# Kernel tuning notes

Measured on AMD Instinct MI355X. Metric: run time of the kernel, lower is better.

## Reference

```python
import jax, jax.numpy as jnp
import numpy as np

N, E, G, DIM = 100000, 1600000, 64, 128
BN_EPS = 1e-5


def setup_inputs() -> dict:
    key = jax.random.key(0)
    ks = jax.random.split(key, 20)
    inp = {
        "x": jax.random.normal(ks[0], (N, DIM), jnp.float32),
        "edge_attr": jax.random.normal(ks[1], (E, DIM), jnp.float32),
        "u": jax.random.normal(ks[2], (G, DIM), jnp.float32),
        "edge_index": jax.random.randint(ks[3], (2, E), 0, N, jnp.int32),
        "batch": jnp.sort(jax.random.randint(ks[4], (N,), 0, G, jnp.int32)),
    }
    # MLP params: layer 0 is Linear(3*DIM, DIM), layers 1,2 are Linear(DIM, DIM)
    def xavier(k, shape):
        fan_in, fan_out = shape[1], shape[0]
        lim = jnp.sqrt(6.0 / (fan_in + fan_out))
        return jax.random.uniform(k, shape, jnp.float32, -lim, lim)
    inp["W0"] = xavier(ks[5], (DIM, 3 * DIM)); inp["b0"] = jnp.zeros((DIM,), jnp.float32)
    inp["W1"] = xavier(ks[6], (DIM, DIM));     inp["b1"] = jnp.zeros((DIM,), jnp.float32)
    inp["W2"] = xavier(ks[7], (DIM, DIM));     inp["b2"] = jnp.zeros((DIM,), jnp.float32)
    for i in range(3):
        inp[f"g{i}"] = jnp.ones((DIM,), jnp.float32)   # BN gamma
        inp[f"bt{i}"] = jnp.zeros((DIM,), jnp.float32)  # BN beta
    return inp


def _bn(h, gamma, beta):
    # training-mode BatchNorm1d: batch mean, biased variance
    mu = jnp.mean(h, axis=0)
    var = jnp.var(h, axis=0)
    return (h - mu) * jax.lax.rsqrt(var + BN_EPS) * gamma + beta


def reference(x, edge_attr, u, W0, b0, W1, b1, W2, b2,
              g0, bt0, g1, bt1, g2, bt2, edge_index, batch):
    n = x.shape[0]
    src = edge_index[0]
    # scatter_mean(edge_attr, src) -> [N, DIM]
    sums = jax.ops.segment_sum(edge_attr, src, num_segments=n)
    cnt = jax.ops.segment_sum(jnp.ones((edge_attr.shape[0],), edge_attr.dtype),
                              src, num_segments=n)
    v_e = sums / jnp.maximum(cnt, 1.0)[:, None]
    out = jnp.concatenate([x, v_e, u[batch]], axis=1)  # [N, 3*DIM]
    for W, b, g, bt in ((W0, b0, g0, bt0), (W1, b1, g1, bt1), (W2, b2, g2, bt2)):
        out = jax.nn.relu(out @ W.T + b)
        out = _bn(out, g, bt)
        # dropout_rate = 0.0 -> identity
    return out
```

## Files before the change

### kernel.cpp

```cpp
#include <hip/hip_runtime.h>

#define DIMF 128
#define CAP 128

typedef __bf16 bf16x8 __attribute__((ext_vector_type(8)));
typedef float f32x4 __attribute__((ext_vector_type(4)));
typedef float f32x2 __attribute__((ext_vector_type(2)));

__device__ __forceinline__ unsigned short f2bf(float f) {
    union { float f; unsigned u; } v; v.f = f;
    unsigned r = v.u + 0x7FFFu + ((v.u >> 16) & 1u);
    return (unsigned short)(r >> 16);
}
__device__ __forceinline__ float bf2f(unsigned short h) {
    union { unsigned u; float f; } v; v.u = ((unsigned)h) << 16; return v.f;
}

__global__ __launch_bounds__(256) void k_zero_wconv(int* __restrict__ zbase, int zints,
                                                    const float* __restrict__ W, unsigned short* __restrict__ Wb,
                                                    int n4) {
    int idx = blockIdx.x * 256 + threadIdx.x;
    int z0 = idx * 2;
    if (z0 + 1 < zints) {
        *reinterpret_cast<int2*>(zbase + z0) = int2{0, 0};
    } else if (z0 < zints) {
        zbase[z0] = 0;
    }
    if (idx < n4) {
        float4 v = *reinterpret_cast<const float4*>(W + (size_t)idx * 4);
        ushort4 o = { f2bf(v.x), f2bf(v.y), f2bf(v.z), f2bf(v.w) };
        *reinterpret_cast<ushort4*>(Wb + (size_t)idx * 4) = o;
    }
}

__global__ __launch_bounds__(256) void k_fillb(const int* __restrict__ src, int* __restrict__ cnt,
                                               int* __restrict__ order, int E) {
    int e = blockIdx.x * 256 + threadIdx.x;
    if (e < E) {
        int s = src[e];
        int p = atomicAdd(&cnt[s], 1);
        if (p < CAP) order[(size_t)s * CAP + p] = e;
    }
}

__global__ __launch_bounds__(256) void k_gather(const float* __restrict__ ea, const int* __restrict__ order,
                                                const int* __restrict__ cnt,
                                                unsigned short* __restrict__ ve, int n) {
    int node = blockIdx.x * 4 + (threadIdx.x >> 6);
    if (node >= n) return;
    int lane = threadIdx.x & 63;
    int c = cnt[node];
    if (c > CAP) c = CAP;
    size_t base = (size_t)node * CAP;

    int id0 = (lane < c) ? order[base + lane] : 0;
    int id1 = (c > 64 && lane < c - 64) ? order[base + 64 + lane] : 0;

    float s0 = 0.f, s1 = 0.f;
    f32x2 cur[8], nxt[8];

    int nb = c >> 3;
    if (nb > 0) {
#pragma unroll
        for (int k = 0; k < 8; ++k) {
            int eid = __shfl(id0, k, 64);
            cur[k] = __builtin_nontemporal_load(reinterpret_cast<const f32x2*>(ea + (size_t)eid * DIMF) + lane);
        }
        for (int b = 1; b < nb; ++b) {
            int j0 = b * 8;
#pragma unroll
            for (int k = 0; k < 8; ++k) {
                int j = j0 + k;
                int eid = (j < 64) ? __shfl(id0, j, 64) : __shfl(id1, j - 64, 64);
                nxt[k] = __builtin_nontemporal_load(reinterpret_cast<const f32x2*>(ea + (size_t)eid * DIMF) + lane);
            }
#pragma unroll
            for (int k = 0; k < 8; ++k) {
                s0 += cur[k][0]; s1 += cur[k][1];
                cur[k] = nxt[k];
            }
        }
#pragma unroll
        for (int k = 0; k < 8; ++k) { s0 += cur[k][0]; s1 += cur[k][1]; }
    }
    for (int j = nb * 8; j < c; ++j) {
        int eid = (j < 64) ? __shfl(id0, j, 64) : __shfl(id1, j - 64, 64);
        f32x2 v = __builtin_nontemporal_load(reinterpret_cast<const f32x2*>(ea + (size_t)eid * DIMF) + lane);
        s0 += v[0]; s1 += v[1];
    }

    float inv = 1.0f / (float)(c > 1 ? c : 1);
    ushort2 o = { f2bf(s0 * inv), f2bf(s1 * inv) };
    *reinterpret_cast<ushort2*>(ve + (size_t)node * DIMF + lane * 2) = o;
}

#define BM 64

__global__ __launch_bounds__(256) void k_gemm0(const float* __restrict__ x,
                                               const unsigned short* __restrict__ ve,
                                               const float* __restrict__ u,
                                               const int* __restrict__ batch,
                                               const unsigned short* __restrict__ W,
                                               const float* __restrict__ bias,
                                               unsigned short* __restrict__ H,
                                               float* __restrict__ st, int rows) {
    __shared__ __align__(16) unsigned short lA[BM][136];
    __shared__ __align__(16) unsigned short lB[DIMF][136];
    __shared__ float sm[DIMF], sq[DIMF];
    __shared__ int sbatch[BM];
    int tid = threadIdx.x;
    int row0 = blockIdx.x * BM;
    if (tid < DIMF) { sm[tid] = 0.f; sq[tid] = 0.f; }
    if (tid < BM) {
        int gr = row0 + tid;
        sbatch[tid] = (gr < rows) ? batch[gr] : 0;
    }

    int lane = tid & 63, wave = tid >> 6;
    int wm = wave >> 1, wn = wave & 1;
    int l15 = lane & 15, l4 = lane >> 4;
    f32x4 acc[2][4] = {};

    int fr = tid >> 5, fc = (tid & 31) * 4;
    int hr = tid >> 4, hc = (tid & 15) * 8;

#pragma unroll
    for (int chunk = 0; chunk < 3; ++chunk) {
        if (chunk == 0) {
#pragma unroll
            for (int i = 0; i < 8; ++i) {
                int r = fr + i * 8;
                int gr = row0 + r;
                float4 v = (gr < rows) ? *reinterpret_cast<const float4*>(x + (size_t)gr * DIMF + fc)
                                       : float4{0.f, 0.f, 0.f, 0.f};
                ushort4 o2 = { f2bf(v.x), f2bf(v.y), f2bf(v.z), f2bf(v.w) };
                *reinterpret_cast<ushort4*>(&lA[r][fc]) = o2;
            }
        } else if (chunk == 1) {
#pragma unroll
            for (int i = 0; i < 4; ++i) {
                int r = hr + i * 16;
                int gr = row0 + r;
                uint4 v = (gr < rows) ? *reinterpret_cast<const uint4*>(ve + (size_t)gr * DIMF + hc)
                                      : uint4{0u, 0u, 0u, 0u};
                *reinterpret_cast<uint4*>(&lA[r][hc]) = v;
            }
        } else {
#pragma unroll
            for (int i = 0; i < 8; ++i) {
                int r = fr + i * 8;
                int gr = row0 + r;
                int b = sbatch[r];
                float4 v = (gr < rows) ? *reinterpret_cast<const float4*>(u + (size_t)b * DIMF + fc)
                                       : float4{0.f, 0.f, 0.f, 0.f};
                ushort4 o2 = { f2bf(v.x), f2bf(v.y), f2bf(v.z), f2bf(v.w) };
                *reinterpret_cast<ushort4*>(&lA[r][fc]) = o2;
            }
        }
#pragma unroll
        for (int i = 0; i < 8; ++i) {
            int r = hr + i * 16;
            uint4 v = *reinterpret_cast<const uint4*>(W + (size_t)r * 384 + chunk * 128 + hc);
            *reinterpret_cast<uint4*>(&lB[r][hc]) = v;
        }
        __syncthreads();
#pragma unroll
        for (int ks = 0; ks < 4; ++ks) {
            bf16x8 af[2], bfr[4];
#pragma unroll
            for (int mi = 0; mi < 2; ++mi)
                af[mi] = *reinterpret_cast<const bf16x8*>(&lA[wm * 32 + mi * 16 + l15][ks * 32 + l4 * 8]);
#pragma unroll
            for (int ni = 0; ni < 4; ++ni)
                bfr[ni] = *reinterpret_cast<const bf16x8*>(&lB[wn * 64 + ni * 16 + l15][ks * 32 + l4 * 8]);
#pragma unroll
            for (int mi = 0; mi < 2; ++mi)
#pragma unroll
                for (int ni = 0; ni < 4; ++ni)
                    acc[mi][ni] = __builtin_amdgcn_mfma_f32_16x16x32_bf16(af[mi], bfr[ni], acc[mi][ni], 0, 0, 0);
        }
        __syncthreads();
    }

#pragma unroll
    for (int mi = 0; mi < 2; ++mi)
#pragma unroll
        for (int ni = 0; ni < 4; ++ni) {
            int c = wn * 64 + ni * 16 + l15;
            float s = 0.f, q = 0.f;
#pragma unroll
            for (int i = 0; i < 4; ++i) {
                int r = row0 + wm * 32 + mi * 16 + l4 * 4 + i;
                if (r < rows) {
                    float z = acc[mi][ni][i] + bias[c];
                    z = fmaxf(z, 0.f);
                    H[(size_t)r * DIMF + c] = f2bf(z);
                    s += z; q += z * z;
                }
            }
            atomicAdd(&sm[c], s);
            atomicAdd(&sq[c], q);
        }
    __syncthreads();
    if (tid < DIMF) { atomicAdd(&st[tid], sm[tid]); atomicAdd(&st[DIMF + tid], sq[tid]); }
}

__global__ __launch_bounds__(256) void k_gemmF(const unsigned short* __restrict__ A,
                                               const float* __restrict__ W,
                                               const float* __restrict__ bn,
                                               const float* __restrict__ stp,
                                               const float* __restrict__ g,
                                               const float* __restrict__ bt,
                                               unsigned short* __restrict__ H,
                                               float* __restrict__ st, int rows) {
    const int K = 128;
    __shared__ __align__(16) unsigned short lA[BM][136];
    __shared__ __align__(16) unsigned short lB[DIMF][136];
    __shared__ float sS[DIMF], sT[DIMF], bb[DIMF], sm[DIMF], sq[DIMF];
    int tid = threadIdx.x;
    int row0 = blockIdx.x * BM;

    if (tid < DIMF) {
        float invn = 1.0f / (float)rows;
        float mu = stp[tid] * invn;
        float var = stp[DIMF + tid] * invn - mu * mu;
        var = var > 0.f ? var : 0.f;
        float sc = rsqrtf(var + 1e-5f) * g[tid];
        sS[tid] = sc;
        sT[tid] = bt[tid] - mu * sc;
        sm[tid] = 0.f; sq[tid] = 0.f;
    }

    int hr = tid >> 4, hc = (tid & 15) * 8;
#pragma unroll
    for (int i = 0; i < 4; ++i) {
        int r = hr + i * 16;
        int gr = row0 + r;
        uint4 v = (gr < rows) ? *reinterpret_cast<const uint4*>(A + (size_t)gr * K + hc)
                              : uint4{0u, 0u, 0u, 0u};
        *reinterpret_cast<uint4*>(&lA[r][hc]) = v;
    }
    __syncthreads();

    int fr = tid >> 5, fc = (tid & 31) * 4;
#pragma unroll
    for (int it = 0; it < 16; ++it) {
        int r = fr + it * 8;
        float4 w = *reinterpret_cast<const float4*>(W + (size_t)r * K + fc);
        ushort4 ob = { f2bf(w.x * sS[fc]), f2bf(w.y * sS[fc + 1]),
                       f2bf(w.z * sS[fc + 2]), f2bf(w.w * sS[fc + 3]) };
        *reinterpret_cast<ushort4*>(&lB[r][fc]) = ob;
        float p = w.x * sT[fc] + w.y * sT[fc + 1] + w.z * sT[fc + 2] + w.w * sT[fc + 3];
#pragma unroll
        for (int m = 16; m > 0; m >>= 1) p += __shfl_xor(p, m, 32);
        if ((tid & 31) == 0) bb[r] = bn[r] + p;
    }
    __syncthreads();

    int lane = tid & 63, wave = tid >> 6;
    int wm = wave >> 1, wn = wave & 1;
    int l15 = lane & 15, l4 = lane >> 4;
    f32x4 acc[2][4] = {};

#pragma unroll
    for (int ks = 0; ks < 4; ++ks) {
        bf16x8 af[2], bfr[4];
#pragma unroll
        for (int mi = 0; mi < 2; ++mi)
            af[mi] = *reinterpret_cast<const bf16x8*>(&lA[wm * 32 + mi * 16 + l15][ks * 32 + l4 * 8]);
#pragma unroll
        for (int ni = 0; ni < 4; ++ni)
            bfr[ni] = *reinterpret_cast<const bf16x8*>(&lB[wn * 64 + ni * 16 + l15][ks * 32 + l4 * 8]);
#pragma unroll
        for (int mi = 0; mi < 2; ++mi)
#pragma unroll
            for (int ni = 0; ni < 4; ++ni)
                acc[mi][ni] = __builtin_amdgcn_mfma_f32_16x16x32_bf16(af[mi], bfr[ni], acc[mi][ni], 0, 0, 0);
    }

#pragma unroll
    for (int mi = 0; mi < 2; ++mi)
#pragma unroll
        for (int ni = 0; ni < 4; ++ni) {
            int c = wn * 64 + ni * 16 + l15;
            float s = 0.f, q = 0.f;
#pragma unroll
            for (int i = 0; i < 4; ++i) {
                int r = row0 + wm * 32 + mi * 16 + l4 * 4 + i;
                if (r < rows) {
                    float z = acc[mi][ni][i] + bb[c];
                    z = fmaxf(z, 0.f);
                    H[(size_t)r * DIMF + c] = f2bf(z);
                    s += z; q += z * z;
                }
            }
            atomicAdd(&sm[c], s);
            atomicAdd(&sq[c], q);
        }
    __syncthreads();
    if (tid < DIMF) { atomicAdd(&st[tid], sm[tid]); atomicAdd(&st[DIMF + tid], sq[tid]); }
}

__global__ __launch_bounds__(256) void k_final(const unsigned short* __restrict__ H, const float* __restrict__ st,
                                               const float* __restrict__ g, const float* __restrict__ bt,
                                               float* __restrict__ out, int n) {
    int idx = blockIdx.x * 256 + threadIdx.x;
    if (idx >= n * 32) return;
    int r = idx >> 5, q = (idx & 31) * 4;
    float invn = 1.0f / (float)n;
    ushort4 h = *reinterpret_cast<const ushort4*>(H + (size_t)r * DIMF + q);
    float hv[4] = { bf2f(h.x), bf2f(h.y), bf2f(h.z), bf2f(h.w) };
    float ov[4];
#pragma unroll
    for (int k = 0; k < 4; ++k) {
        int c = q + k;
        float mu = st[c] * invn;
        float var = st[DIMF + c] * invn - mu * mu;
        var = var > 0.f ? var : 0.f;
        float sc = rsqrtf(var + 1e-5f) * g[c];
        ov[k] = hv[k] * sc + (bt[c] - mu * sc);
    }
    float4 o = { ov[0], ov[1], ov[2], ov[3] };
    *reinterpret_cast<float4*>(out + (size_t)r * DIMF + q) = o;
}

extern "C" void kernel_launch(void* const* d_in, const int* in_sizes, int n_in,
                              void* d_out, int out_size, void* d_ws, size_t ws_size,
                              hipStream_t stream) {
    const float* x   = (const float*)d_in[0];
    const float* ea  = (const float*)d_in[1];
    const float* u   = (const float*)d_in[2];
    const int* eidx  = (const int*)d_in[3];
    const int* batch = (const int*)d_in[4];
    const float* W0  = (const float*)d_in[5];
    const float* b0  = (const float*)d_in[6];
    const float* W1  = (const float*)d_in[7];
    const float* b1  = (const float*)d_in[8];
    const float* W2  = (const float*)d_in[9];
    const float* b2  = (const float*)d_in[10];
    const float* g0  = (const float*)d_in[11];
    const float* bt0 = (const float*)d_in[12];
    const float* g1  = (const float*)d_in[13];
    const float* bt1 = (const float*)d_in[14];
    const float* g2  = (const float*)d_in[15];
    const float* bt2 = (const float*)d_in[16];

    int N = in_sizes[0] / DIMF;
    int E = in_sizes[1] / DIMF;
    const int* src = eidx;

    char* base = (char*)d_ws;
    size_t o = 0;
    auto alloc = [&](size_t sz) { size_t p = o; o = (o + sz + 255) & ~(size_t)255; return p; };
    size_t off_cnt   = alloc((size_t)N * 4);
    size_t off_st    = alloc(3 * 256 * 4);
    size_t off_order = alloc((size_t)N * CAP * 4);
    size_t off_W0b   = alloc((size_t)DIMF * 384 * 2);
    size_t off_ve    = alloc((size_t)N * DIMF * 2);
    size_t off_h0    = alloc((size_t)N * DIMF * 2);
    size_t off_h1    = alloc((size_t)N * DIMF * 2);
    size_t off_h2    = alloc((size_t)N * DIMF * 2);

    int* cnt        = (int*)(base + off_cnt);
    float* st       = (float*)(base + off_st);
    int* order      = (int*)(base + off_order);
    unsigned short* W0b = (unsigned short*)(base + off_W0b);
    unsigned short* ve = (unsigned short*)(base + off_ve);
    unsigned short* h0 = (unsigned short*)(base + off_h0);
    unsigned short* h1 = (unsigned short*)(base + off_h1);
    unsigned short* h2 = (unsigned short*)(base + off_h2);
    float* outp = (float*)d_out;

    int zints = (int)((off_st + 3 * 256 * 4) / 4);
    int EB = (E + 255) / 256;
    int NQ = (N * 32 + 255) / 256;
    int GB = (N + BM - 1) / BM;
    int GG = (N + 3) / 4;

    k_zero_wconv<<<256, 256, 0, stream>>>((int*)base, zints, W0, W0b, DIMF * 384 / 4);
    k_fillb<<<EB, 256, 0, stream>>>(src, cnt, order, E);
    k_gather<<<GG, 256, 0, stream>>>(ea, order, cnt, ve, N);

    k_gemm0<<<GB, 256, 0, stream>>>(x, ve, u, batch, W0b, b0, h0, st, N);
    k_gemmF<<<GB, 256, 0, stream>>>(h0, W1, b1, st, g0, bt0, h1, st + 256, N);
    k_gemmF<<<GB, 256, 0, stream>>>(h1, W2, b2, st + 256, g1, bt1, h2, st + 512, N);
    k_final<<<NQ, 256, 0, stream>>>(h2, st + 512, g2, bt2, outp, N);
}
```

Baseline: 586.3 us.

## Scatter edge features as bf16 into per-node slots before gather-reduce

Replaces the index-bucketing pass plus random-row gather with a pass that reads each edge row once, converts it to bf16, and writes it into a per-node slot buffer chosen by an atomic counter. The gather kernel then reads contiguous bf16 rows per node and sums them with half-wave lane pairs. The bucket cap is also lowered from 128 to 64. The aim is to make the edge reads streaming instead of random, at the cost of a large scattered bf16 write and extra rounding of edge features. The lower cap would drop edges if any node has more than 64.

After: 655.3 us. 1.12x slower.

```diff
diff --git a/kernel.cpp b/kernel.cpp
--- a/kernel.cpp
+++ b/kernel.cpp
@@ -1,7 +1,7 @@
 #include <hip/hip_runtime.h>
 
 #define DIMF 128
-#define CAP 128
+#define CAP 64
 
 typedef __bf16 bf16x8 __attribute__((ext_vector_type(8)));
 typedef float f32x4 __attribute__((ext_vector_type(4)));
@@ -14,6 +14,9 @@
 }
 __device__ __forceinline__ float bf2f(unsigned short h) {
     union { unsigned u; float f; } v; v.u = ((unsigned)h) << 16; return v.f;
+}
+__device__ __forceinline__ float uasf(unsigned u) {
+    union { unsigned u; float f; } v; v.u = u; return v.f;
 }
 
 __global__ __launch_bounds__(256) void k_zero_wconv(int* __restrict__ zbase, int zints,
@@ -33,65 +36,93 @@
     }
 }
 
-__global__ __launch_bounds__(256) void k_fillb(const int* __restrict__ src, int* __restrict__ cnt,
-                                               int* __restrict__ order, int E) {
-    int e = blockIdx.x * 256 + threadIdx.x;
-    if (e < E) {
-        int s = src[e];
-        int p = atomicAdd(&cnt[s], 1);
-        if (p < CAP) order[(size_t)s * CAP + p] = e;
-    }
-}
-
-__global__ __launch_bounds__(256) void k_gather(const float* __restrict__ ea, const int* __restrict__ order,
+__global__ __launch_bounds__(256) void k_perm(const float* __restrict__ ea, const int* __restrict__ src,
+                                              int* __restrict__ cnt, unsigned short* __restrict__ eab, int E) {
+    int wv = blockIdx.x * 4 + (threadIdx.x >> 6);
+    int lane = threadIdx.x & 63;
+    int e0 = wv * 4;
+    if (e0 >= E) return;
+
+    int e_l = e0 + lane;
+    int sv = -1, pv = 0;
+    if (lane < 4 && e_l < E) {
+        sv = src[e_l];
+        pv = atomicAdd(&cnt[sv], 1);
+    }
+
+    f32x2 v[4];
+#pragma unroll
+    for (int k = 0; k < 4; ++k) {
+        int e = e0 + k;
+        if (e < E)
+            v[k] = __builtin_nontemporal_load(reinterpret_cast<const f32x2*>(ea + (size_t)e * DIMF) + lane);
+    }
+#pragma unroll
+    for (int k = 0; k < 4; ++k) {
+        int e = e0 + k;
+        if (e < E) {
+            int s = __shfl(sv, k, 64);
+            int p = __shfl(pv, k, 64);
+            if (p < CAP) {
+                ushort2 o = { f2bf(v[k][0]), f2bf(v[k][1]) };
+                *(reinterpret_cast<ushort2*>(eab + ((size_t)s * CAP + p) * DIMF) + lane) = o;
+            }
+        }
+    }
+}
+
+__global__ __launch_bounds__(256) void k_gather(const unsigned short* __restrict__ eab,
                                                 const int* __restrict__ cnt,
                                                 unsigned short* __restrict__ ve, int n) {
     int node = blockIdx.x * 4 + (threadIdx.x >> 6);
     if (node >= n) return;
     int lane = threadIdx.x & 63;
+    int l32 = lane & 31;
     int c = cnt[node];
     if (c > CAP) c = CAP;
-    size_t base = (size_t)node * CAP;
-
-    int id0 = (lane < c) ? order[base + lane] : 0;
-    int id1 = (c > 64 && lane < c - 64) ? order[base + 64 + lane] : 0;
-
-    float s0 = 0.f, s1 = 0.f;
-    f32x2 cur[8], nxt[8];
-
-    int nb = c >> 3;
+    const unsigned* base = reinterpret_cast<const unsigned*>(eab + (size_t)node * CAP * DIMF);
+
+    float s0 = 0.f, s1 = 0.f, s2 = 0.f, s3 = 0.f;
+    uint2 cur[8], nxt[8];
+    int np = c >> 1;
+
+#define LDP(i) (*reinterpret_cast<const uint2*>(base + (size_t)(i) * 128 + lane * 2))
+#define ACCP(w) { s0 += uasf((w).x << 16); s1 += uasf((w).x & 0xffff0000u); \
+                  s2 += uasf((w).y << 16); s3 += uasf((w).y & 0xffff0000u); }
+
+    int nb = np >> 3;
     if (nb > 0) {
 #pragma unroll
-        for (int k = 0; k < 8; ++k) {
-            int eid = __shfl(id0, k, 64);
-            cur[k] = __builtin_nontemporal_load(reinterpret_cast<const f32x2*>(ea + (size_t)eid * DIMF) + lane);
-        }
+        for (int k = 0; k < 8; ++k) cur[k] = LDP(k);
         for (int b = 1; b < nb; ++b) {
-            int j0 = b * 8;
-#pragma unroll
-            for (int k = 0; k < 8; ++k) {
-                int j = j0 + k;
-                int eid = (j < 64) ? __shfl(id0, j, 64) : __shfl(id1, j - 64, 64);
-                nxt[k] = __builtin_nontemporal_load(reinterpret_cast<const f32x2*>(ea + (size_t)eid * DIMF) + lane);
-            }
-#pragma unroll
-            for (int k = 0; k < 8; ++k) {
-                s0 += cur[k][0]; s1 += cur[k][1];
-                cur[k] = nxt[k];
-            }
-        }
-#pragma unroll
-        for (int k = 0; k < 8; ++k) { s0 += cur[k][0]; s1 += cur[k][1]; }
-    }
-    for (int j = nb * 8; j < c; ++j) {
-        int eid = (j < 64) ? __shfl(id0, j, 64) : __shfl(id1, j - 64, 64);
-        f32x2 v = __builtin_nontemporal_load(reinterpret_cast<const f32x2*>(ea + (size_t)eid * DIMF) + lane);
-        s0 += v[0]; s1 += v[1];
-    }
-
-    float inv = 1.0f / (float)(c > 1 ? c : 1);
-    ushort2 o = { f2bf(s0 * inv), f2bf(s1 * inv) };
-    *reinterpret_cast<ushort2*>(ve + (size_t)node * DIMF + lane * 2) = o;
+#pragma unroll
+            for (int k = 0; k < 8; ++k) nxt[k] = LDP(b * 8 + k);
+#pragma unroll
+            for (int k = 0; k < 8; ++k) { ACCP(cur[k]); cur[k] = nxt[k]; }
+        }
+#pragma unroll
+        for (int k = 0; k < 8; ++k) ACCP(cur[k]);
+    }
+    for (int i = nb * 8; i < np; ++i) { uint2 w = LDP(i); ACCP(w); }
+    if (c & 1) {
+        if (lane < 32) {
+            uint2 w = *reinterpret_cast<const uint2*>(base + (size_t)(c - 1) * 64 + l32 * 2);
+            ACCP(w);
+        }
+    }
+#undef LDP
+#undef ACCP
+
+    s0 += __shfl_xor(s0, 32, 64);
+    s1 += __shfl_xor(s1, 32, 64);
+    s2 += __shfl_xor(s2, 32, 64);
+    s3 += __shfl_xor(s3, 32, 64);
+
+    if (lane < 32) {
+        float inv = 1.0f / (float)(c > 1 ? c : 1);
+        ushort4 o = { f2bf(s0 * inv), f2bf(s1 * inv), f2bf(s2 * inv), f2bf(s3 * inv) };
+        *reinterpret_cast<ushort4*>(ve + (size_t)node * DIMF + l32 * 4) = o;
+    }
 }
 
 #define BM 64
@@ -354,32 +385,32 @@
     auto alloc = [&](size_t sz) { size_t p = o; o = (o + sz + 255) & ~(size_t)255; return p; };
     size_t off_cnt   = alloc((size_t)N * 4);
     size_t off_st    = alloc(3 * 256 * 4);
-    size_t off_order = alloc((size_t)N * CAP * 4);
     size_t off_W0b   = alloc((size_t)DIMF * 384 * 2);
     size_t off_ve    = alloc((size_t)N * DIMF * 2);
     size_t off_h0    = alloc((size_t)N * DIMF * 2);
     size_t off_h1    = alloc((size_t)N * DIMF * 2);
     size_t off_h2    = alloc((size_t)N * DIMF * 2);
+    size_t off_eab   = alloc((size_t)N * CAP * DIMF * 2);
 
     int* cnt        = (int*)(base + off_cnt);
     float* st       = (float*)(base + off_st);
-    int* order      = (int*)(base + off_order);
     unsigned short* W0b = (unsigned short*)(base + off_W0b);
-    unsigned short* ve = (unsigned short*)(base + off_ve);
-    unsigned short* h0 = (unsigned short*)(base + off_h0);
-    unsigned short* h1 = (unsigned short*)(base + off_h1);
-    unsigned short* h2 = (unsigned short*)(base + off_h2);
+    unsigned short* ve  = (unsigned short*)(base + off_ve);
+    unsigned short* h0  = (unsigned short*)(base + off_h0);
+    unsigned short* h1  = (unsigned short*)(base + off_h1);
+    unsigned short* h2  = (unsigned short*)(base + off_h2);
+    unsigned short* eab = (unsigned short*)(base + off_eab);
     float* outp = (float*)d_out;
 
     int zints = (int)((off_st + 3 * 256 * 4) / 4);
-    int EB = (E + 255) / 256;
     int NQ = (N * 32 + 255) / 256;
     int GB = (N + BM - 1) / BM;
     int GG = (N + 3) / 4;
+    int PB = (E + 15) / 16;
 
     k_zero_wconv<<<256, 256, 0, stream>>>((int*)base, zints, W0, W0b, DIMF * 384 / 4);
-    k_fillb<<<EB, 256, 0, stream>>>(src, cnt, order, E);
-    k_gather<<<GG, 256, 0, stream>>>(ea, order, cnt, ve, N);
+    k_perm<<<PB, 256, 0, stream>>>(ea, src, cnt, eab, E);
+    k_gather<<<GG, 256, 0, stream>>>(eab, cnt, ve, N);
 
     k_gemm0<<<GB, 256, 0, stream>>>(x, ve, u, batch, W0b, b0, h0, st, N);
     k_gemmF<<<GB, 256, 0, stream>>>(h0, W1, b1, st, g0, bt0, h1, st + 256, N);
```

## Replace bucketed edge gather with atomic scatter-add into fp32 node sums

Applied to the files above, without the earlier changes.

Drops the per-node order list and gather kernel. Each wave now streams edge rows sequentially and atomically adds them into an fp32 node-sum buffer, and a separate pass divides by counts and converts to bf16. This removes the index bucketing and the random row reads, and no longer truncates at a per-node cap. In exchange it issues one float atomic per element and adds a memset plus an extra write and read of a full fp32 node buffer.

Result: slower. 1.669 ms (+184.7%).

```diff
diff --git a/kernel.cpp b/kernel.cpp
--- a/kernel.cpp
+++ b/kernel.cpp
@@ -1,7 +1,6 @@
 #include <hip/hip_runtime.h>
 
 #define DIMF 128
-#define CAP 128
 
 typedef __bf16 bf16x8 __attribute__((ext_vector_type(8)));
 typedef float f32x4 __attribute__((ext_vector_type(4)));
@@ -33,65 +32,44 @@
     }
 }
 
-__global__ __launch_bounds__(256) void k_fillb(const int* __restrict__ src, int* __restrict__ cnt,
-                                               int* __restrict__ order, int E) {
-    int e = blockIdx.x * 256 + threadIdx.x;
-    if (e < E) {
-        int s = src[e];
-        int p = atomicAdd(&cnt[s], 1);
-        if (p < CAP) order[(size_t)s * CAP + p] = e;
-    }
-}
-
-__global__ __launch_bounds__(256) void k_gather(const float* __restrict__ ea, const int* __restrict__ order,
-                                                const int* __restrict__ cnt,
-                                                unsigned short* __restrict__ ve, int n) {
-    int node = blockIdx.x * 4 + (threadIdx.x >> 6);
-    if (node >= n) return;
+__global__ __launch_bounds__(256) void k_edge(const float* __restrict__ ea, const int* __restrict__ src,
+                                              float* __restrict__ vsum, int* __restrict__ cnt, int E) {
+    int nw = gridDim.x * 4;
+    int wv = blockIdx.x * 4 + (threadIdx.x >> 6);
     int lane = threadIdx.x & 63;
-    int c = cnt[node];
-    if (c > CAP) c = CAP;
-    size_t base = (size_t)node * CAP;
-
-    int id0 = (lane < c) ? order[base + lane] : 0;
-    int id1 = (c > 64 && lane < c - 64) ? order[base + 64 + lane] : 0;
-
-    float s0 = 0.f, s1 = 0.f;
-    f32x2 cur[8], nxt[8];
-
-    int nb = c >> 3;
-    if (nb > 0) {
-#pragma unroll
-        for (int k = 0; k < 8; ++k) {
-            int eid = __shfl(id0, k, 64);
-            cur[k] = __builtin_nontemporal_load(reinterpret_cast<const f32x2*>(ea + (size_t)eid * DIMF) + lane);
-        }
-        for (int b = 1; b < nb; ++b) {
-            int j0 = b * 8;
-#pragma unroll
-            for (int k = 0; k < 8; ++k) {
-                int j = j0 + k;
-                int eid = (j < 64) ? __shfl(id0, j, 64) : __shfl(id1, j - 64, 64);
-                nxt[k] = __builtin_nontemporal_load(reinterpret_cast<const f32x2*>(ea + (size_t)eid * DIMF) + lane);
-            }
-#pragma unroll
-            for (int k = 0; k < 8; ++k) {
-                s0 += cur[k][0]; s1 += cur[k][1];
-                cur[k] = nxt[k];
-            }
-        }
-#pragma unroll
-        for (int k = 0; k < 8; ++k) { s0 += cur[k][0]; s1 += cur[k][1]; }
-    }
-    for (int j = nb * 8; j < c; ++j) {
-        int eid = (j < 64) ? __shfl(id0, j, 64) : __shfl(id1, j - 64, 64);
-        f32x2 v = __builtin_nontemporal_load(reinterpret_cast<const f32x2*>(ea + (size_t)eid * DIMF) + lane);
-        s0 += v[0]; s1 += v[1];
-    }
-
+    for (int e0 = wv * 4; e0 < E; e0 += nw * 4) {
+        f32x2 v[4]; int s[4];
+#pragma unroll
+        for (int k = 0; k < 4; ++k) {
+            int e = e0 + k;
+            if (e < E) {
+                v[k] = __builtin_nontemporal_load(reinterpret_cast<const f32x2*>(ea + (size_t)e * DIMF) + lane);
+                s[k] = src[e];
+            }
+        }
+#pragma unroll
+        for (int k = 0; k < 4; ++k) {
+            int e = e0 + k;
+            if (e < E) {
+                float* dst = vsum + (size_t)s[k] * DIMF + lane * 2;
+                atomicAdd(dst, v[k][0]);
+                atomicAdd(dst + 1, v[k][1]);
+                if (lane == 0) atomicAdd(&cnt[s[k]], 1);
+            }
+        }
+    }
+}
+
+__global__ __launch_bounds__(256) void k_ve(const float* __restrict__ vsum, const int* __restrict__ cnt,
+                                            unsigned short* __restrict__ ve, int n) {
+    int idx = blockIdx.x * 256 + threadIdx.x;
+    if (idx >= n * 32) return;
+    int r = idx >> 5, q = (idx & 31) * 4;
+    int c = cnt[r];
     float inv = 1.0f / (float)(c > 1 ? c : 1);
-    ushort2 o = { f2bf(s0 * inv), f2bf(s1 * inv) };
-    *reinterpret_cast<ushort2*>(ve + (size_t)node * DIMF + lane * 2) = o;
+    float4 v = *reinterpret_cast<const float4*>(vsum + (size_t)r * DIMF + q);
+    ushort4 o = { f2bf(v.x * inv), f2bf(v.y * inv), f2bf(v.z * inv), f2bf(v.w * inv) };
+    *reinterpret_cast<ushort4*>(ve + (size_t)r * DIMF + q) = o;
 }
 
 #define BM 64
@@ -354,32 +332,32 @@
     auto alloc = [&](size_t sz) { size_t p = o; o = (o + sz + 255) & ~(size_t)255; return p; };
     size_t off_cnt   = alloc((size_t)N * 4);
     size_t off_st    = alloc(3 * 256 * 4);
-    size_t off_order = alloc((size_t)N * CAP * 4);
     size_t off_W0b   = alloc((size_t)DIMF * 384 * 2);
     size_t off_ve    = alloc((size_t)N * DIMF * 2);
     size_t off_h0    = alloc((size_t)N * DIMF * 2);
     size_t off_h1    = alloc((size_t)N * DIMF * 2);
     size_t off_h2    = alloc((size_t)N * DIMF * 2);
+    size_t off_vsum  = alloc((size_t)N * DIMF * 4);
 
     int* cnt        = (int*)(base + off_cnt);
     float* st       = (float*)(base + off_st);
-    int* order      = (int*)(base + off_order);
     unsigned short* W0b = (unsigned short*)(base + off_W0b);
-    unsigned short* ve = (unsigned short*)(base + off_ve);
-    unsigned short* h0 = (unsigned short*)(base + off_h0);
-    unsigned short* h1 = (unsigned short*)(base + off_h1);
-    unsigned short* h2 = (unsigned short*)(base + off_h2);
+    unsigned short* ve  = (unsigned short*)(base + off_ve);
+    unsigned short* h0  = (unsigned short*)(base + off_h0);
+    unsigned short* h1  = (unsigned short*)(base + off_h1);
+    unsigned short* h2  = (unsigned short*)(base + off_h2);
+    float* vsum     = (float*)(base + off_vsum);
     float* outp = (float*)d_out;
 
     int zints = (int)((off_st + 3 * 256 * 4) / 4);
-    int EB = (E + 255) / 256;
     int NQ = (N * 32 + 255) / 256;
     int GB = (N + BM - 1) / BM;
-    int GG = (N + 3) / 4;
 
     k_zero_wconv<<<256, 256, 0, stream>>>((int*)base, zints, W0, W0b, DIMF * 384 / 4);
-    k_fillb<<<EB, 256, 0, stream>>>(src, cnt, order, E);
-    k_gather<<<GG, 256, 0, stream>>>(ea, order, cnt, ve, N);
+    hipMemsetAsync(vsum, 0, (size_t)N * DIMF * 4, stream);
+
+    k_edge<<<4096, 256, 0, stream>>>(ea, src, vsum, cnt, E);
+    k_ve<<<NQ, 256, 0, stream>>>(vsum, cnt, ve, N);
 
     k_gemm0<<<GB, 256, 0, stream>>>(x, ve, u, batch, W0b, b0, h0, st, N);
     k_gemmF<<<GB, 256, 0, stream>>>(h0, W1, b1, st, g0, bt0, h1, st + 256, N);
```
